# Kernel optimization log

Hardware: AMD Instinct MI355X
Metric: run time of the kernel (lower is better)

## Reference

```python
import jax, jax.numpy as jnp
import numpy as np

EPS_W = 1e-8   # weight reciprocal eps (matches torch code)
EPS_BN = 1e-5  # torch BatchNorm1d default eps


def _cdist(a, b):
    # a: [B,N,3], b: [B,M,3] -> [B,N,M] euclidean distances
    sq = (jnp.sum(a * a, -1)[:, :, None] + jnp.sum(b * b, -1)[:, None, :]
          - 2.0 * jnp.einsum('bnd,bmd->bnm', a, b))
    return jnp.sqrt(jnp.maximum(sq, 0.0))


def _bn_relu(x, gamma, beta):
    # x: [B,C,N]; training-mode batch norm over (B,N)
    mean = jnp.mean(x, axis=(0, 2), keepdims=True)
    var = jnp.mean((x - mean) ** 2, axis=(0, 2), keepdims=True)
    y = (x - mean) * jax.lax.rsqrt(var + EPS_BN)
    y = y * gamma[None, :, None] + beta[None, :, None]
    return jax.nn.relu(y)


def setup_inputs() -> dict:
    key = jax.random.key(0)
    ks = jax.random.split(key, 8)
    B, Np, Ns = 16, 1024, 4096
    Cp, Cs, Co = 256, 128, 256
    return {
        'xyz_prev': jax.random.normal(ks[0], (B, Np, 3), jnp.float32),
        'xyz_skip': jax.random.normal(ks[1], (B, Ns, 3), jnp.float32),
        'points_prev': jax.random.normal(ks[2], (B, Cp, Np), jnp.float32),
        'points_skip': jax.random.normal(ks[3], (B, Cs, Ns), jnp.float32),
        'W1': jax.random.normal(ks[4], (Co, Cp + Cs), jnp.float32) * 0.05,
        'g1': jnp.ones((Co,), jnp.float32),
        'b1': jnp.zeros((Co,), jnp.float32),
        'W2': jax.random.normal(ks[5], (Co, Co), jnp.float32) * 0.05,
        'g2': jnp.ones((Co,), jnp.float32),
        'b2': jnp.zeros((Co,), jnp.float32),
    }


def reference(xyz_prev, xyz_skip, points_prev, points_skip, W1, g1, b1, W2, g2, b2):
    dist = _cdist(xyz_skip, xyz_prev)                       # [B,Ns,Np]
    neg, idx = jax.lax.top_k(-dist, 3)                      # 3 smallest dists
    dist_recip = 1.0 / (dist + EPS_W)
    # NOTE: normalization is over ALL N_prev points (faithful to source)
    weight = dist_recip / jnp.sum(dist_recip, axis=2, keepdims=True)
    w3 = jnp.take_along_axis(weight, idx, axis=2)           # [B,Ns,3]
    pp = jnp.swapaxes(points_prev, 1, 2)                    # [B,Np,Cp]
    g = jnp.take_along_axis(pp[:, None, :, :], idx[..., None], axis=2)  # [B,Ns,3,Cp]
    interp = jnp.einsum('bnk,bnkc->bcn', w3, g)             # [B,Cp,Ns]
    x = jnp.concatenate([interp, points_skip], axis=1)      # [B,Cp+Cs,Ns]
    x = _bn_relu(jnp.einsum('bcn,oc->bon', x, W1), g1, b1)
    x = _bn_relu(jnp.einsum('bcn,oc->bon', x, W2), g2, b2)
    return x
```

## Files before the change

kernel.cpp:

```cpp
#include <hip/hip_runtime.h>
#include <math.h>

constexpr int NB  = 16;
constexpr int NP  = 1024;
constexpr int NS  = 4096;
constexpr int CP  = 256;
constexpr int CS  = 128;
constexpr int CIN = 384;
constexpr int CO  = 256;

constexpr int NCHUNK = 16;
constexpr int CHPTS  = NP / NCHUNK;

typedef unsigned int uint;
typedef unsigned short ushort_t;
typedef __attribute__((ext_vector_type(8))) short short8;
typedef __attribute__((ext_vector_type(8))) unsigned short us8;
typedef __attribute__((ext_vector_type(4))) float f32x4;

__device__ __forceinline__ ushort_t f2bf(float f) {
  uint u = __float_as_uint(f);
  uint r = (u + 0x7fffu + ((u >> 16) & 1u)) >> 16;
  return (ushort_t)r;
}
__device__ __forceinline__ float bf2f(ushort_t u) {
  return __uint_as_float(((uint)u) << 16);
}

__device__ __forceinline__ void gload16(const void* g, void* l) {
  __builtin_amdgcn_global_load_lds(
      (const __attribute__((address_space(1))) uint*)g,
      (__attribute__((address_space(3))) uint*)l, 16, 0, 0);
}

__device__ __forceinline__ void tkp(float pxv, float pyv, float pzv, int pi,
                                    float qx, float qy, float qz,
                                    float& k0, float& k1, float& k2,
                                    float& rsum) {
  float dx = pxv - qx, dy = pyv - qy, dz = pzv - qz;
  float sq = fmaf(dz, dz, fmaf(dy, dy, fmaf(dx, dx, 1e-16f)));
  rsum += __builtin_amdgcn_rsqf(sq);
  float k = __uint_as_float((__float_as_uint(sq) & 0xFFFFFC00u) | (uint)pi);
  k2 = __builtin_amdgcn_fmed3f(k1, k2, k);
  k1 = __builtin_amdgcn_fmed3f(k0, k1, k);
  k0 = fminf(k0, k);
}

__global__ __launch_bounds__(256) void topk_chunk_kernel(
    const float* __restrict__ xyz_prev, const float* __restrict__ xyz_skip,
    float* __restrict__ pbuf) {
  __shared__ float px[CHPTS], py[CHPTS], pz[CHPTS];
  int q  = blockIdx.y;
  int b  = blockIdx.z;
  int tid = threadIdx.x;
  if (tid < CHPTS) {
    const float* xp = xyz_prev + ((size_t)b * NP + q * CHPTS + tid) * 3;
    px[tid] = xp[0]; py[tid] = xp[1]; pz[tid] = xp[2];
  }
  __syncthreads();
  int nA = blockIdx.x * 512 + tid;
  int nB = nA + 256;
  const float* xqA = xyz_skip + ((size_t)b * NS + nA) * 3;
  const float* xqB = xyz_skip + ((size_t)b * NS + nB) * 3;
  float qxA = xqA[0], qyA = xqA[1], qzA = xqA[2];
  float qxB = xqB[0], qyB = xqB[1], qzB = xqB[2];
  float kA0 = INFINITY, kA1 = INFINITY, kA2 = INFINITY;
  float kB0 = INFINITY, kB1 = INFINITY, kB2 = INFINITY;
  float rsA = 0.f, rsB = 0.f;
  int pbase = q * CHPTS;
  for (int p = 0; p < CHPTS; p += 4) {
    float4 X = *(const float4*)&px[p];
    float4 Y = *(const float4*)&py[p];
    float4 Z = *(const float4*)&pz[p];
    tkp(X.x, Y.x, Z.x, pbase + p + 0, qxA, qyA, qzA, kA0, kA1, kA2, rsA);
    tkp(X.x, Y.x, Z.x, pbase + p + 0, qxB, qyB, qzB, kB0, kB1, kB2, rsB);
    tkp(X.y, Y.y, Z.y, pbase + p + 1, qxA, qyA, qzA, kA0, kA1, kA2, rsA);
    tkp(X.y, Y.y, Z.y, pbase + p + 1, qxB, qyB, qzB, kB0, kB1, kB2, rsB);
    tkp(X.z, Y.z, Z.z, pbase + p + 2, qxA, qyA, qzA, kA0, kA1, kA2, rsA);
    tkp(X.z, Y.z, Z.z, pbase + p + 2, qxB, qyB, qzB, kB0, kB1, kB2, rsB);
    tkp(X.w, Y.w, Z.w, pbase + p + 3, qxA, qyA, qzA, kA0, kA1, kA2, rsA);
    tkp(X.w, Y.w, Z.w, pbase + p + 3, qxB, qyB, qzB, kB0, kB1, kB2, rsB);
  }
  size_t PA = ((size_t)(b * NCHUNK + q) * NS + nA) * 4;
  size_t PB = ((size_t)(b * NCHUNK + q) * NS + nB) * 4;
  *(float4*)(pbuf + PA) = make_float4(kA0, kA1, kA2, rsA);
  *(float4*)(pbuf + PB) = make_float4(kB0, kB1, kB2, rsB);
}

__global__ __launch_bounds__(256) void topk_merge_kernel(
    const float* __restrict__ pbuf, float* __restrict__ w3,
    int* __restrict__ idx3) {
  int gid = blockIdx.x * 256 + threadIdx.x;
  int b = gid >> 12;
  int n = gid & (NS - 1);
  float k0 = INFINITY, k1 = INFINITY, k2 = INFINITY;
  float rsum = 0.f;
  #pragma unroll 4
  for (int q = 0; q < NCHUNK; q++) {
    float4 v = *(const float4*)(pbuf + ((size_t)(b * NCHUNK + q) * NS + n) * 4);
    rsum += v.w;
    k2 = __builtin_amdgcn_fmed3f(k1, k2, v.x);
    k1 = __builtin_amdgcn_fmed3f(k0, k1, v.x);
    k0 = fminf(k0, v.x);
    k2 = __builtin_amdgcn_fmed3f(k1, k2, v.y);
    k1 = __builtin_amdgcn_fmed3f(k0, k1, v.y);
    k0 = fminf(k0, v.y);
    k2 = __builtin_amdgcn_fmed3f(k1, k2, v.z);
    k1 = __builtin_amdgcn_fmed3f(k0, k1, v.z);
    k0 = fminf(k0, v.z);
  }
  float inv = 1.0f / rsum;
  uint u0 = __float_as_uint(k0), u1 = __float_as_uint(k1), u2 = __float_as_uint(k2);
  float d0 = __uint_as_float(u0 & 0xFFFFFC00u);
  float d1 = __uint_as_float(u1 & 0xFFFFFC00u);
  float d2 = __uint_as_float(u2 & 0xFFFFFC00u);
  size_t base = (size_t)gid * 3;
  w3[base + 0] = __builtin_amdgcn_rsqf(d0) * inv;
  w3[base + 1] = __builtin_amdgcn_rsqf(d1) * inv;
  w3[base + 2] = __builtin_amdgcn_rsqf(d2) * inv;
  idx3[base + 0] = (int)(u0 & 1023u);
  idx3[base + 1] = (int)(u1 & 1023u);
  idx3[base + 2] = (int)(u2 & 1023u);
}

__global__ __launch_bounds__(256) void wcast_kernel(
    const float* __restrict__ W1, const float* __restrict__ W2,
    ushort_t* __restrict__ W1b, ushort_t* __restrict__ W2b,
    float* __restrict__ st1, float* __restrict__ st2) {
  int tid = threadIdx.x;
  if (blockIdx.x == 0) {
    st1[tid] = 0.f; st1[tid + 256] = 0.f;
    st2[tid] = 0.f; st2[tid + 256] = 0.f;
  }
  int t = blockIdx.x * 256 + tid;
  int n1 = CO * CIN / 4;
  if (t < n1) {
    float4 v = *(const float4*)(W1 + t * 4);
    ushort4 o; o.x = f2bf(v.x); o.y = f2bf(v.y); o.z = f2bf(v.z); o.w = f2bf(v.w);
    *(ushort4*)(W1b + t * 4) = o;
  } else {
    int u = t - n1;
    float4 v = *(const float4*)(W2 + u * 4);
    ushort4 o; o.x = f2bf(v.x); o.y = f2bf(v.y); o.z = f2bf(v.z); o.w = f2bf(v.w);
    *(ushort4*)(W2b + u * 4) = o;
  }
}

__global__ __launch_bounds__(256) void ppT_kernel(
    const float* __restrict__ pp, ushort_t* __restrict__ pptT) {
  __shared__ float tl[64][65];
  int p0 = blockIdx.x * 64, c0 = blockIdx.y * 64, b = blockIdx.z;
  int tid = threadIdx.x;
  const float* P = pp + (size_t)b * CP * NP;
  int pi4 = (tid & 15) * 4, ci = tid >> 4;
  #pragma unroll
  for (int r = 0; r < 4; r++) {
    int cc = ci + 16 * r;
    float4 v = *(const float4*)(P + (size_t)(c0 + cc) * NP + p0 + pi4);
    tl[cc][pi4] = v.x; tl[cc][pi4 + 1] = v.y; tl[cc][pi4 + 2] = v.z; tl[cc][pi4 + 3] = v.w;
  }
  __syncthreads();
  ushort_t* O = pptT + (size_t)b * NP * CP;
  int ci4 = (tid & 15) * 4, pi = tid >> 4;
  #pragma unroll
  for (int r = 0; r < 4; r++) {
    int pr = pi + 16 * r;
    ushort4 o;
    o.x = f2bf(tl[ci4 + 0][pr]); o.y = f2bf(tl[ci4 + 1][pr]);
    o.z = f2bf(tl[ci4 + 2][pr]); o.w = f2bf(tl[ci4 + 3][pr]);
    *(ushort4*)(O + (size_t)(p0 + pr) * CP + c0 + ci4) = o;
  }
}

__global__ __launch_bounds__(256) void skipT_kernel(
    const float* __restrict__ sk, ushort_t* __restrict__ xsk) {
  __shared__ float tl[64][65];
  int n0 = blockIdx.x * 64, c0 = blockIdx.y * 64, b = blockIdx.z;
  int tid = threadIdx.x;
  const float* S = sk + (size_t)b * CS * NS;
  int ni4 = (tid & 15) * 4, ci = tid >> 4;
  #pragma unroll
  for (int r = 0; r < 4; r++) {
    int cc = ci + 16 * r;
    float4 v = *(const float4*)(S + (size_t)(c0 + cc) * NS + n0 + ni4);
    tl[cc][ni4] = v.x; tl[cc][ni4 + 1] = v.y; tl[cc][ni4 + 2] = v.z; tl[cc][ni4 + 3] = v.w;
  }
  __syncthreads();
  ushort_t* O = xsk + (size_t)b * NS * CS;
  int ci4 = (tid & 15) * 4, ni = tid >> 4;
  #pragma unroll
  for (int r = 0; r < 4; r++) {
    int nr = ni + 16 * r;
    ushort4 o;
    o.x = f2bf(tl[ci4 + 0][nr]); o.y = f2bf(tl[ci4 + 1][nr]);
    o.z = f2bf(tl[ci4 + 2][nr]); o.w = f2bf(tl[ci4 + 3][nr]);
    *(ushort4*)(O + (size_t)(n0 + nr) * CS + c0 + ci4) = o;
  }
}

template <int MODE>
__global__ __launch_bounds__(256) void gemm_fused_kernel(
    const ushort_t* __restrict__ Xsrc,
    const ushort_t* __restrict__ xsk,
    const float* __restrict__ w3, const int* __restrict__ idx3,
    const ushort_t* __restrict__ Wb, ushort_t* __restrict__ Yb,
    float* __restrict__ stats,
    const float* __restrict__ stats_in, const float* __restrict__ g_in,
    const float* __restrict__ bt_in) {
  constexpr int KD = (MODE == 0) ? CIN : CO;
  constexpr int NT = KD / 32;
  __shared__ __align__(16) char lds_raw[33792];
  ushort_t* ldsX = (ushort_t*)lds_raw;
  ushort_t* ldsW = (ushort_t*)(lds_raw + 8192);
  __shared__ float ssum[128], ssq[128];
  __shared__ float a1s[MODE ? CO : 1], s1s[MODE ? CO : 1];

  int tid = threadIdx.x;
  int w = tid >> 6, l = tid & 63;
  int bid = blockIdx.x;
  int by = (bid >> 3) & 1;
  int s  = (bid & 7) + 8 * (bid >> 4);
  int bx = s & 31;
  int bz = s >> 5;
  int n0 = bx * 128;
  if (tid < 128) { ssum[tid] = 0.f; ssq[tid] = 0.f; }
  if constexpr (MODE == 1) {
    float cnt = (float)NB * (float)NS;
    float m = stats_in[tid] / cnt;
    float var = stats_in[CO + tid] / cnt - m * m;
    var = fmaxf(var, 0.f);
    float invs = rsqrtf(var + 1e-5f);
    float av = g_in[tid] * invs;
    a1s[tid] = av; s1s[tid] = bt_in[tid] - m * av;
  }
  __syncthreads();

  int r = tid >> 1, h = tid & 1;
  int sw = (r >> 1) & 3;
  int p0c = 2 * h, p1c = 2 * h + 1;
  int cl0 = (p0c ^ sw) * 8, cl1 = (p1c ^ sw) * 8;
  int j0 = 0, j1 = 0, j2 = 0; float w0 = 0.f, w1 = 0.f, w2 = 0.f;
  const ushort_t* Pb = nullptr; const ushort_t* Kb = nullptr;
  const ushort_t* Xb = nullptr;
  if constexpr (MODE == 0) {
    size_t nb3 = ((size_t)bz * NS + n0 + r) * 3;
    j0 = idx3[nb3 + 0]; j1 = idx3[nb3 + 1]; j2 = idx3[nb3 + 2];
    w0 = w3[nb3 + 0]; w1 = w3[nb3 + 1]; w2 = w3[nb3 + 2];
    Pb = Xsrc + (size_t)bz * NP * CP;
    Kb = xsk + ((size_t)bz * NS + n0 + r) * CS;
  } else {
    Xb = Xsrc + ((size_t)bz * NS + n0 + r) * KD;
  }
  int wrb = w * 16 + (l >> 2);
  int wcl = l & 3;
  int wksw = 8 * (wcl ^ ((wrb >> 1) & 3));

  us8 ra0, rb0, rc0, ra1, rb1, rc1;
  us8 rg0, rg1;

  auto issue = [&](int tt) {
    int cb = tt * 32;
    if constexpr (MODE == 0) {
      if (cb < CP) {
        ra0 = *(const us8*)(Pb + (size_t)j0 * CP + cb + cl0);
        rb0 = *(const us8*)(Pb + (size_t)j1 * CP + cb + cl0);
        rc0 = *(const us8*)(Pb + (size_t)j2 * CP + cb + cl0);
        ra1 = *(const us8*)(Pb + (size_t)j0 * CP + cb + cl1);
        rb1 = *(const us8*)(Pb + (size_t)j1 * CP + cb + cl1);
        rc1 = *(const us8*)(Pb + (size_t)j2 * CP + cb + cl1);
      } else {
        rg0 = *(const us8*)(Kb + cb - CP + cl0);
        rg1 = *(const us8*)(Kb + cb - CP + cl1);
      }
    } else {
      rg0 = *(const us8*)(Xb + cb + cl0);
      rg1 = *(const us8*)(Xb + cb + cl1);
    }
    ushort_t* wdst = ldsW + (tt & 1) * (128 * 32);
    int ks = cb + wksw;
    gload16(Wb + (size_t)(by * 128 + wrb) * KD + ks, &wdst[(w * 16) * 32]);
    gload16(Wb + (size_t)(by * 128 + 64 + wrb) * KD + ks, &wdst[(64 + w * 16) * 32]);
  };

  f32x4 acc[4][4];
  #pragma unroll
  for (int i = 0; i < 4; i++)
    #pragma unroll
    for (int j = 0; j < 4; j++) acc[i][j] = {0.f, 0.f, 0.f, 0.f};

  int wn = (w & 1) * 64, wo = (w >> 1) * 64;
  int lr = l & 15, lk = l >> 4;

  issue(0);

  #pragma unroll
  for (int t = 0; t < NT; t++) {
    {
      us8 v0, v1;
      if constexpr (MODE == 0) {
        if (t * 32 < CP) {
          #pragma unroll
          for (int e = 0; e < 8; e++) {
            v0[e] = f2bf(w0 * bf2f(ra0[e]) + w1 * bf2f(rb0[e]) + w2 * bf2f(rc0[e]));
            v1[e] = f2bf(w0 * bf2f(ra1[e]) + w1 * bf2f(rb1[e]) + w2 * bf2f(rc1[e]));
          }
        } else { v0 = rg0; v1 = rg1; }
      } else {
        int c0l = t * 32 + cl0, c1l = t * 32 + cl1;
        float4 a0 = *(const float4*)&a1s[c0l], a0b = *(const float4*)&a1s[c0l + 4];
        float4 s0 = *(const float4*)&s1s[c0l], s0b = *(const float4*)&s1s[c0l + 4];
        float4 a1v = *(const float4*)&a1s[c1l], a1b = *(const float4*)&a1s[c1l + 4];
        float4 s1v = *(const float4*)&s1s[c1l], s1b = *(const float4*)&s1s[c1l + 4];
        const float* a0p = (const float*)&a0; const float* a0bp = (const float*)&a0b;
        const float* s0p = (const float*)&s0; const float* s0bp = (const float*)&s0b;
        const float* a1p = (const float*)&a1v; const float* a1bp = (const float*)&a1b;
        const float* s1p = (const float*)&s1v; const float* s1bp = (const float*)&s1b;
        #pragma unroll
        for (int e = 0; e < 4; e++) {
          v0[e]     = f2bf(fmaxf(fmaf(a0p[e],  bf2f(rg0[e]),     s0p[e]),  0.f));
          v0[e + 4] = f2bf(fmaxf(fmaf(a0bp[e], bf2f(rg0[e + 4]), s0bp[e]), 0.f));
          v1[e]     = f2bf(fmaxf(fmaf(a1p[e],  bf2f(rg1[e]),     s1p[e]),  0.f));
          v1[e + 4] = f2bf(fmaxf(fmaf(a1bp[e], bf2f(rg1[e + 4]), s1bp[e]), 0.f));
        }
      }
      *(us8*)&ldsX[r * 32 + p0c * 8] = v0;
      *(us8*)&ldsX[r * 32 + p1c * 8] = v1;
    }
    if (t + 1 < NT) issue(t + 1);
    if constexpr (MODE == 0) {
      if (t + 1 < 8)        asm volatile("s_waitcnt vmcnt(8) lgkmcnt(0)" ::: "memory");
      else if (t + 1 < NT)  asm volatile("s_waitcnt vmcnt(4) lgkmcnt(0)" ::: "memory");
      else                  asm volatile("s_waitcnt vmcnt(0) lgkmcnt(0)" ::: "memory");
    } else {
      if (t + 1 < NT)       asm volatile("s_waitcnt vmcnt(4) lgkmcnt(0)" ::: "memory");
      else                  asm volatile("s_waitcnt vmcnt(0) lgkmcnt(0)" ::: "memory");
    }
    __builtin_amdgcn_s_barrier();
    __builtin_amdgcn_sched_barrier(0);
    {
      const ushort_t* Wl = ldsW + (t & 1) * (128 * 32);
      short8 af[4], bf_[4];
      #pragma unroll
      for (int i = 0; i < 4; i++) {
        int rr = wn + i * 16 + lr;
        int cs = lk ^ ((rr >> 1) & 3);
        af[i] = *(const short8*)&ldsX[rr * 32 + cs * 8];
      }
      #pragma unroll
      for (int j = 0; j < 4; j++) {
        int rr = wo + j * 16 + lr;
        int cs = lk ^ ((rr >> 1) & 3);
        bf_[j] = *(const short8*)&Wl[rr * 32 + cs * 8];
      }
      __builtin_amdgcn_s_setprio(1);
      #pragma unroll
      for (int i = 0; i < 4; i++)
        #pragma unroll
        for (int j = 0; j < 4; j++)
          acc[i][j] = __builtin_amdgcn_mfma_f32_16x16x32_bf16(af[i], bf_[j], acc[i][j], 0, 0, 0);
      __builtin_amdgcn_s_setprio(0);
    }
    __builtin_amdgcn_s_barrier();
    __builtin_amdgcn_sched_barrier(0);
  }

  #pragma unroll
  for (int j = 0; j < 4; j++) {
    int ol = wo + j * 16 + lr;
    float ps = 0.f, pq = 0.f;
    #pragma unroll
    for (int i = 0; i < 4; i++)
      #pragma unroll
      for (int rg = 0; rg < 4; rg++) { float v = acc[i][j][rg]; ps += v; pq += v * v; }
    atomicAdd(&ssum[ol], ps);
    atomicAdd(&ssq[ol], pq);
  }
  ushort_t* lout = (ushort_t*)lds_raw;
  #pragma unroll
  for (int i = 0; i < 4; i++)
    #pragma unroll
    for (int j = 0; j < 4; j++)
      #pragma unroll
      for (int rg = 0; rg < 4; rg++) {
        int nl = wn + i * 16 + lk * 4 + rg;
        int ol = wo + j * 16 + lr;
        lout[nl * 132 + ol] = f2bf(acc[i][j][rg]);
      }
  __syncthreads();
  {
    int row = tid >> 1, half = tid & 1;
    const ushort_t* src = lout + row * 132 + half * 64;
    ushort_t* dst = Yb + ((size_t)bz * NS + n0 + row) * CO + by * 128 + half * 64;
    #pragma unroll
    for (int k = 0; k < 8; k++)
      *(us8*)(dst + k * 8) = *(const us8*)(src + k * 8);
  }
  if (tid < 128) {
    atomicAdd(&stats[by * 128 + tid], ssum[tid]);
    atomicAdd(&stats[CO + by * 128 + tid], ssq[tid]);
  }
}

__global__ __launch_bounds__(256) void bnrelu_tr_kernel(
    const ushort_t* __restrict__ y2b, const float* __restrict__ stats_in,
    const float* __restrict__ g_in, const float* __restrict__ bt_in,
    float* __restrict__ out) {
  __shared__ float tl[64][65];
  __shared__ float a2s[64], s2s[64];
  int n0 = blockIdx.x * 64, o0 = blockIdx.y * 64, b = blockIdx.z;
  const ushort_t* Y = y2b + (size_t)b * NS * CO;
  int tid = threadIdx.x;
  if (tid < 64) {
    int o = o0 + tid;
    float cnt = (float)NB * (float)NS;
    float m = stats_in[o] / cnt;
    float var = stats_in[CO + o] / cnt - m * m;
    var = fmaxf(var, 0.f);
    float invs = rsqrtf(var + 1e-5f);
    float av = g_in[o] * invs;
    a2s[tid] = av; s2s[tid] = bt_in[o] - m * av;
  }
  int o8 = (tid & 7) * 8, row = tid >> 3;
  #pragma unroll
  for (int r = 0; r < 2; r++) {
    int ii = row + 32 * r;
    const ushort_t* src = Y + (size_t)(n0 + ii) * CO + o0 + o8;
    ushort4 v0 = *(const ushort4*)(src);
    ushort4 v1 = *(const ushort4*)(src + 4);
    tl[ii][o8 + 0] = bf2f(v0.x); tl[ii][o8 + 1] = bf2f(v0.y);
    tl[ii][o8 + 2] = bf2f(v0.z); tl[ii][o8 + 3] = bf2f(v0.w);
    tl[ii][o8 + 4] = bf2f(v1.x); tl[ii][o8 + 5] = bf2f(v1.y);
    tl[ii][o8 + 6] = bf2f(v1.z); tl[ii][o8 + 7] = bf2f(v1.w);
  }
  __syncthreads();
  float* O = out + (size_t)b * CO * NS;
  int ii4 = (tid & 15) * 4, j = tid >> 4;
  #pragma unroll
  for (int r = 0; r < 4; r++) {
    int jj = j + 16 * r;
    float av = a2s[jj], sv = s2s[jj];
    float4 v;
    v.x = fmaxf(fmaf(av, tl[ii4 + 0][jj], sv), 0.f);
    v.y = fmaxf(fmaf(av, tl[ii4 + 1][jj], sv), 0.f);
    v.z = fmaxf(fmaf(av, tl[ii4 + 2][jj], sv), 0.f);
    v.w = fmaxf(fmaf(av, tl[ii4 + 3][jj], sv), 0.f);
    *(float4*)(O + (size_t)(o0 + jj) * NS + n0 + ii4) = v;
  }
}

extern "C" void kernel_launch(void* const* d_in, const int* in_sizes, int n_in,
                              void* d_out, int out_size, void* d_ws, size_t ws_size,
                              hipStream_t stream) {
  const float* xyz_prev    = (const float*)d_in[0];
  const float* xyz_skip    = (const float*)d_in[1];
  const float* points_prev = (const float*)d_in[2];
  const float* points_skip = (const float*)d_in[3];
  const float* W1 = (const float*)d_in[4];
  const float* g1 = (const float*)d_in[5];
  const float* b1 = (const float*)d_in[6];
  const float* W2 = (const float*)d_in[7];
  const float* g2 = (const float*)d_in[8];
  const float* b2 = (const float*)d_in[9];
  float* out = (float*)d_out;

  char* W = (char*)d_ws;
  size_t off = 0;
  auto alloc = [&](size_t bytes) {
    size_t o = off; off = (off + bytes + 255) & ~(size_t)255; return o;
  };
  ushort_t* xsk  = (ushort_t*)(W + alloc((size_t)NB * NS * CS * 2));
  ushort_t* y1b  = (ushort_t*)(W + alloc((size_t)NB * NS * CO * 2));
  ushort_t* pptT = (ushort_t*)(W + alloc((size_t)NB * NP * CP * 2));
  ushort_t* W1b  = (ushort_t*)(W + alloc((size_t)CO * CIN * 2));
  ushort_t* W2b  = (ushort_t*)(W + alloc((size_t)CO * CO * 2));
  float* w3   = (float*)(W + alloc((size_t)NB * NS * 3 * 4));
  int*   idx3 = (int*)(W + alloc((size_t)NB * NS * 3 * 4));
  float* st1  = (float*)(W + alloc(512 * 4));
  float* st2  = (float*)(W + alloc(512 * 4));
  size_t y2_off = alloc((size_t)NB * NS * CO * 2);
  bool full = (ws_size >= off);
  ushort_t* y2b = full ? (ushort_t*)(W + y2_off) : (ushort_t*)d_out;
  float* pbuf = full ? (float*)(W + y2_off) : (float*)d_out;

  hipLaunchKernelGGL(topk_chunk_kernel, dim3(NS / 512, NCHUNK, NB), dim3(256), 0,
                     stream, xyz_prev, xyz_skip, pbuf);
  hipLaunchKernelGGL(topk_merge_kernel, dim3(NB * NS / 256), dim3(256), 0, stream,
                     pbuf, w3, idx3);
  hipLaunchKernelGGL(wcast_kernel, dim3((CO * CIN / 4 + CO * CO / 4 + 255) / 256),
                     dim3(256), 0, stream, W1, W2, W1b, W2b, st1, st2);
  hipLaunchKernelGGL(ppT_kernel, dim3(NP / 64, CP / 64, NB), dim3(256), 0, stream,
                     points_prev, pptT);
  hipLaunchKernelGGL(skipT_kernel, dim3(NS / 64, CS / 64, NB), dim3(256), 0, stream,
                     points_skip, xsk);
  hipLaunchKernelGGL((gemm_fused_kernel<0>), dim3(1024), dim3(256), 0, stream,
                     pptT, xsk, w3, idx3, W1b, y1b, st1,
                     (const float*)nullptr, (const float*)nullptr,
                     (const float*)nullptr);
  hipLaunchKernelGGL((gemm_fused_kernel<1>), dim3(1024), dim3(256), 0, stream,
                     y1b, (const ushort_t*)nullptr, (const float*)nullptr,
                     (const int*)nullptr, W2b, y2b, st2, st1, g1, b1);
  if (full) {
    hipLaunchKernelGGL(bnrelu_tr_kernel, dim3(NS / 64, CO / 64, NB), dim3(256), 0,
                       stream, y2b, st2, g2, b2, out);
  } else {
    float* stage = (float*)d_ws;
    hipLaunchKernelGGL(bnrelu_tr_kernel, dim3(NS / 64, CO / 64, NB), dim3(256), 0,
                       stream, y2b, st2, g2, b2, stage);
    hipMemcpyAsync(out, stage, (size_t)NB * NS * CO * 4, hipMemcpyDeviceToDevice,
                   stream);
  }
}
```

Before: 160.3 us.

## Deepen GEMM pipeline with 4-slot LDS ring and register triple-buffering

```diff
diff --git a/kernel.cpp b/kernel.cpp
--- a/kernel.cpp
+++ b/kernel.cpp
@@ -209,9 +209,8 @@
     const float* __restrict__ bt_in) {
   constexpr int KD = (MODE == 0) ? CIN : CO;
   constexpr int NT = KD / 32;
-  __shared__ __align__(16) char lds_raw[33792];
-  ushort_t* ldsX = (ushort_t*)lds_raw;
-  ushort_t* ldsW = (ushort_t*)(lds_raw + 8192);
+  constexpr int TILE = 8192;
+  __shared__ __align__(16) char lds_raw[65536];
   __shared__ float ssum[128], ssq[128];
   __shared__ float a1s[MODE ? CO : 1], s1s[MODE ? CO : 1];
 
@@ -255,31 +254,59 @@
   int wcl = l & 3;
   int wksw = 8 * (wcl ^ ((wrb >> 1) & 3));
 
-  us8 ra0, rb0, rc0, ra1, rb1, rc1;
-  us8 rg0, rg1;
-
-  auto issue = [&](int tt) {
+  us8 xr[3][MODE == 0 ? 6 : 2];
+
+  auto issueX = [&](int tt) {
     int cb = tt * 32;
+    int sl = tt % 3;
     if constexpr (MODE == 0) {
       if (cb < CP) {
-        ra0 = *(const us8*)(Pb + (size_t)j0 * CP + cb + cl0);
-        rb0 = *(const us8*)(Pb + (size_t)j1 * CP + cb + cl0);
-        rc0 = *(const us8*)(Pb + (size_t)j2 * CP + cb + cl0);
-        ra1 = *(const us8*)(Pb + (size_t)j0 * CP + cb + cl1);
-        rb1 = *(const us8*)(Pb + (size_t)j1 * CP + cb + cl1);
-        rc1 = *(const us8*)(Pb + (size_t)j2 * CP + cb + cl1);
+        xr[sl][0] = *(const us8*)(Pb + (size_t)j0 * CP + cb + cl0);
+        xr[sl][1] = *(const us8*)(Pb + (size_t)j1 * CP + cb + cl0);
+        xr[sl][2] = *(const us8*)(Pb + (size_t)j2 * CP + cb + cl0);
+        xr[sl][3] = *(const us8*)(Pb + (size_t)j0 * CP + cb + cl1);
+        xr[sl][4] = *(const us8*)(Pb + (size_t)j1 * CP + cb + cl1);
+        xr[sl][5] = *(const us8*)(Pb + (size_t)j2 * CP + cb + cl1);
       } else {
-        rg0 = *(const us8*)(Kb + cb - CP + cl0);
-        rg1 = *(const us8*)(Kb + cb - CP + cl1);
+        xr[sl][0] = *(const us8*)(Kb + cb - CP + cl0);
+        xr[sl][1] = *(const us8*)(Kb + cb - CP + cl1);
       }
     } else {
-      rg0 = *(const us8*)(Xb + cb + cl0);
-      rg1 = *(const us8*)(Xb + cb + cl1);
+      xr[sl][0] = *(const us8*)(Xb + cb + cl0);
+      xr[sl][1] = *(const us8*)(Xb + cb + cl1);
     }
-    ushort_t* wdst = ldsW + (tt & 1) * (128 * 32);
-    int ks = cb + wksw;
+  };
+  auto issueW = [&](int tt) {
+    ushort_t* wdst = (ushort_t*)(lds_raw + 32768 + (tt & 3) * TILE);
+    int ks = tt * 32 + wksw;
     gload16(Wb + (size_t)(by * 128 + wrb) * KD + ks, &wdst[(w * 16) * 32]);
-    gload16(Wb + (size_t)(by * 128 + 64 + wrb) * KD + ks, &wdst[(64 + w * 16) * 32]);
+    gload16(Wb + (size_t)(by * 128 + 64 + wrb) * KD + ks,
+            &wdst[(64 + w * 16) * 32]);
+  };
+  auto stage = [&](int tt) {
+    int sl = tt % 3;
+    ushort_t* dX = (ushort_t*)(lds_raw + (tt & 3) * TILE);
+    us8 v0, v1;
+    if constexpr (MODE == 0) {
+      if (tt * 32 < CP) {
+        #pragma unroll
+        for (int e = 0; e < 8; e++) {
+          v0[e] = f2bf(w0 * bf2f(xr[sl][0][e]) + w1 * bf2f(xr[sl][1][e]) +
+                       w2 * bf2f(xr[sl][2][e]));
+          v1[e] = f2bf(w0 * bf2f(xr[sl][3][e]) + w1 * bf2f(xr[sl][4][e]) +
+                       w2 * bf2f(xr[sl][5][e]));
+        }
+      } else { v0 = xr[sl][0]; v1 = xr[sl][1]; }
+    } else {
+      int c0l = tt * 32 + cl0, c1l = tt * 32 + cl1;
+      #pragma unroll
+      for (int e = 0; e < 8; e++) {
+        v0[e] = f2bf(fmaxf(fmaf(a1s[c0l + e], bf2f(xr[sl][0][e]), s1s[c0l + e]), 0.f));
+        v1[e] = f2bf(fmaxf(fmaf(a1s[c1l + e], bf2f(xr[sl][1][e]), s1s[c1l + e]), 0.f));
+      }
+    }
+    *(us8*)&dX[r * 32 + p0c * 8] = v0;
+    *(us8*)&dX[r * 32 + p1c * 8] = v1;
   };
 
   f32x4 acc[4][4];
@@ -291,79 +318,53 @@
   int wn = (w & 1) * 64, wo = (w >> 1) * 64;
   int lr = l & 15, lk = l >> 4;
 
-  issue(0);
+  issueX(0); issueX(1); issueW(0); issueX(2); issueW(1);
+  stage(0);
 
   #pragma unroll
   for (int t = 0; t < NT; t++) {
-    {
-      us8 v0, v1;
-      if constexpr (MODE == 0) {
-        if (t * 32 < CP) {
-          #pragma unroll
-          for (int e = 0; e < 8; e++) {
-            v0[e] = f2bf(w0 * bf2f(ra0[e]) + w1 * bf2f(rb0[e]) + w2 * bf2f(rc0[e]));
-            v1[e] = f2bf(w0 * bf2f(ra1[e]) + w1 * bf2f(rb1[e]) + w2 * bf2f(rc1[e]));
-          }
-        } else { v0 = rg0; v1 = rg1; }
-      } else {
-        int c0l = t * 32 + cl0, c1l = t * 32 + cl1;
-        float4 a0 = *(const float4*)&a1s[c0l], a0b = *(const float4*)&a1s[c0l + 4];
-        float4 s0 = *(const float4*)&s1s[c0l], s0b = *(const float4*)&s1s[c0l + 4];
-        float4 a1v = *(const float4*)&a1s[c1l], a1b = *(const float4*)&a1s[c1l + 4];
-        float4 s1v = *(const float4*)&s1s[c1l], s1b = *(const float4*)&s1s[c1l + 4];
-        const float* a0p = (const float*)&a0; const float* a0bp = (const float*)&a0b;
-        const float* s0p = (const float*)&s0; const float* s0bp = (const float*)&s0b;
-        const float* a1p = (const float*)&a1v; const float* a1bp = (const float*)&a1b;
-        const float* s1p = (const float*)&s1v; const float* s1bp = (const float*)&s1b;
-        #pragma unroll
-        for (int e = 0; e < 4; e++) {
-          v0[e]     = f2bf(fmaxf(fmaf(a0p[e],  bf2f(rg0[e]),     s0p[e]),  0.f));
-          v0[e + 4] = f2bf(fmaxf(fmaf(a0bp[e], bf2f(rg0[e + 4]), s0bp[e]), 0.f));
-          v1[e]     = f2bf(fmaxf(fmaf(a1p[e],  bf2f(rg1[e]),     s1p[e]),  0.f));
-          v1[e + 4] = f2bf(fmaxf(fmaf(a1bp[e], bf2f(rg1[e + 4]), s1bp[e]), 0.f));
-        }
-      }
-      *(us8*)&ldsX[r * 32 + p0c * 8] = v0;
-      *(us8*)&ldsX[r * 32 + p1c * 8] = v1;
-    }
-    if (t + 1 < NT) issue(t + 1);
-    if constexpr (MODE == 0) {
-      if (t + 1 < 8)        asm volatile("s_waitcnt vmcnt(8) lgkmcnt(0)" ::: "memory");
-      else if (t + 1 < NT)  asm volatile("s_waitcnt vmcnt(4) lgkmcnt(0)" ::: "memory");
-      else                  asm volatile("s_waitcnt vmcnt(0) lgkmcnt(0)" ::: "memory");
-    } else {
-      if (t + 1 < NT)       asm volatile("s_waitcnt vmcnt(4) lgkmcnt(0)" ::: "memory");
-      else                  asm volatile("s_waitcnt vmcnt(0) lgkmcnt(0)" ::: "memory");
-    }
+    if (t + 1 < NT) stage(t + 1);
+    if (t + 3 < NT) issueX(t + 3);
+    if (t + 2 < NT) issueW(t + 2);
+    int nw = ((t + 2 < NT) ? ((MODE == 0 && t + 2 < 8) ? 6 : 2) : 0)
+           + ((t + 1 < NT) ? 2 : 0)
+           + ((t + 3 < NT) ? ((MODE == 0 && t + 3 < 8) ? 6 : 2) : 0)
+           + ((t + 2 < NT) ? 2 : 0);
+    if (nw >= 16)      asm volatile("s_waitcnt vmcnt(16) lgkmcnt(0)" ::: "memory");
+    else if (nw >= 12) asm volatile("s_waitcnt vmcnt(12) lgkmcnt(0)" ::: "memory");
+    else if (nw >= 8)  asm volatile("s_waitcnt vmcnt(8) lgkmcnt(0)" ::: "memory");
+    else if (nw >= 6)  asm volatile("s_waitcnt vmcnt(6) lgkmcnt(0)" ::: "memory");
+    else if (nw >= 2)  asm volatile("s_waitcnt vmcnt(2) lgkmcnt(0)" ::: "memory");
+    else               asm volatile("s_waitcnt vmcnt(0) lgkmcnt(0)" ::: "memory");
     __builtin_amdgcn_s_barrier();
     __builtin_amdgcn_sched_barrier(0);
     {
-      const ushort_t* Wl = ldsW + (t & 1) * (128 * 32);
-      short8 af[4], bf_[4];
+      const ushort_t* cX = (const ushort_t*)(lds_raw + (t & 3) * TILE);
+      const ushort_t* cW = (const ushort_t*)(lds_raw + 32768 + (t & 3) * TILE);
+      short8 af[4], bfr[4];
       #pragma unroll
       for (int i = 0; i < 4; i++) {
         int rr = wn + i * 16 + lr;
         int cs = lk ^ ((rr >> 1) & 3);
-        af[i] = *(const short8*)&ldsX[rr * 32 + cs * 8];
+        af[i] = *(const short8*)&cX[rr * 32 + cs * 8];
       }
       #pragma unroll
       for (int j = 0; j < 4; j++) {
         int rr = wo + j * 16 + lr;
         int cs = lk ^ ((rr >> 1) & 3);
-        bf_[j] = *(const short8*)&Wl[rr * 32 + cs * 8];
+        bfr[j] = *(const short8*)&cW[rr * 32 + cs * 8];
       }
       __builtin_amdgcn_s_setprio(1);
       #pragma unroll
       for (int i = 0; i < 4; i++)
         #pragma unroll
         for (int j = 0; j < 4; j++)
-          acc[i][j] = __builtin_amdgcn_mfma_f32_16x16x32_bf16(af[i], bf_[j], acc[i][j], 0, 0, 0);
+          acc[i][j] = __builtin_amdgcn_mfma_f32_16x16x32_bf16(af[i], bfr[j], acc[i][j], 0, 0, 0);
       __builtin_amdgcn_s_setprio(0);
     }
-    __builtin_amdgcn_s_barrier();
-    __builtin_amdgcn_sched_barrier(0);
-  }
-
+  }
+
+  __syncthreads();
   #pragma unroll
   for (int j = 0; j < 4; j++) {
     int ol = wo + j * 16 + lr;
@@ -384,12 +385,12 @@
       for (int rg = 0; rg < 4; rg++) {
         int nl = wn + i * 16 + lk * 4 + rg;
         int ol = wo + j * 16 + lr;
-        lout[nl * 132 + ol] = f2bf(acc[i][j][rg]);
+        lout[nl * 136 + ol] = f2bf(acc[i][j][rg]);
       }
   __syncthreads();
   {
     int row = tid >> 1, half = tid & 1;
-    const ushort_t* src = lout + row * 132 + half * 64;
+    const ushort_t* src = lout + row * 136 + half * 64;
     ushort_t* dst = Yb + ((size_t)bz * NS + n0 + row) * CO + by * 128 + half * 64;
     #pragma unroll
     for (int k = 0; k < 8; k++)
```

Result: no change. 161.9 us (+1.0%).
